# Performance work log

Hardware: AMD Instinct MI355X
Metric: run time of the kernel (lower is better)

Reference implementation:

```python
import jax, jax.numpy as jnp
import numpy as np

EMBED = 1024
HEADS = 16
HD = EMBED // HEADS
FF = 4096
EPS = 1e-5

def _layernorm(x, g, b):
    mu = jnp.mean(x, axis=-1, keepdims=True)
    var = jnp.mean(jnp.square(x - mu), axis=-1, keepdims=True)
    return (x - mu) * jax.lax.rsqrt(var + EPS) * g + b

def setup_inputs() -> dict:
    key = jax.random.key(0)
    ks = jax.random.split(key, 10)
    s = 0.02
    return {
        "x": jax.random.normal(ks[0], (4, 2048, EMBED), dtype=jnp.float32),
        "Wq": jax.random.normal(ks[1], (EMBED, EMBED), dtype=jnp.float32) * s,
        "Wk": jax.random.normal(ks[2], (EMBED, EMBED), dtype=jnp.float32) * s,
        "Wv": jax.random.normal(ks[3], (EMBED, EMBED), dtype=jnp.float32) * s,
        "Wo": jax.random.normal(ks[4], (EMBED, EMBED), dtype=jnp.float32) * s,
        "bo": jnp.zeros((EMBED,), dtype=jnp.float32),
        "W1": jax.random.normal(ks[5], (EMBED, FF), dtype=jnp.float32) * s,
        "b1": jnp.zeros((FF,), dtype=jnp.float32),
        "W2": jax.random.normal(ks[6], (FF, EMBED), dtype=jnp.float32) * s,
        "b2": jnp.zeros((EMBED,), dtype=jnp.float32),
        "g1": jnp.ones((EMBED,), dtype=jnp.float32),
        "be1": jnp.zeros((EMBED,), dtype=jnp.float32),
        "g2": jnp.ones((EMBED,), dtype=jnp.float32),
        "be2": jnp.zeros((EMBED,), dtype=jnp.float32),
    }

def reference(x, Wq, Wk, Wv, Wo, bo, W1, b1, W2, b2, g1, be1, g2, be2):
    B, T, _ = x.shape
    # --- pre-norm self-attention (dropout = identity in eval) ---
    h = _layernorm(x, g1, be1)
    q = (h @ Wq).reshape(B, T, HEADS, HD).transpose(0, 2, 1, 3)  # bhtd
    k = (h @ Wk).reshape(B, T, HEADS, HD).transpose(0, 2, 1, 3)
    v = (h @ Wv).reshape(B, T, HEADS, HD).transpose(0, 2, 1, 3)
    scores = jnp.einsum('bhid,bhjd->bhij', q, k) / jnp.sqrt(jnp.float32(HD))
    causal = jnp.tril(jnp.ones((T, T), dtype=bool))
    scores = jnp.where(causal[None, None], scores, -jnp.inf)
    attn = jax.nn.softmax(scores, axis=-1)
    out = jnp.einsum('bhij,bhjd->bhid', attn, v)
    out = out.transpose(0, 2, 1, 3).reshape(B, T, EMBED)
    out = out @ Wo + bo
    x = x + out
    # --- pre-norm GELU FFN ---
    h2 = _layernorm(x, g2, be2)
    ff = jax.nn.gelu(h2 @ W1 + b1, approximate=False) @ W2 + b2
    return x + ff
```

## Files before the change

kernel.cpp:

```cpp
#include <hip/hip_runtime.h>

typedef unsigned short u16;
typedef __attribute__((ext_vector_type(8))) short bf16x8;
typedef __attribute__((ext_vector_type(4))) float f32x4;

#define EMBED 1024
#define FFDIM 4096
#define SEQ   2048
#define NTOK  8192
#define ATT_C 0.18033688011112042f

__device__ __forceinline__ u16 f2bf(float f) {
  union { float f; unsigned int u; } c; c.f = f;
  unsigned int r = ((c.u >> 16) & 1u) + 0x7fffu;
  return (u16)((c.u + r) >> 16);
}

__device__ __forceinline__ unsigned cvtpk(float lo, float hi) {
  unsigned r;
  asm("v_cvt_pk_bf16_f32 %0, %1, %2" : "=v"(r) : "v"(lo), "v"(hi));
  return r;
}

__device__ __forceinline__ void gload16(const u16* g, u16* l) {
  __builtin_amdgcn_global_load_lds((const __attribute__((address_space(1))) void*)g,
                                   (__attribute__((address_space(3))) void*)l, 16, 0, 0);
}

__global__ __launch_bounds__(256) void wtrans(const float* __restrict__ W,
                                              u16* __restrict__ Wt, int K, int N) {
  __shared__ float tile[32][33];
  const int tx = threadIdx.x & 31, ty = threadIdx.x >> 5;
  const int n0 = blockIdx.x << 5, k0 = blockIdx.y << 5;
#pragma unroll
  for (int r = 0; r < 32; r += 8)
    tile[ty + r][tx] = W[(size_t)(k0 + ty + r) * N + n0 + tx];
  __syncthreads();
#pragma unroll
  for (int r = 0; r < 32; r += 8)
    Wt[(size_t)(n0 + ty + r) * K + k0 + tx] = f2bf(tile[tx][ty + r]);
}

__global__ __launch_bounds__(256) void vtrans(const u16* __restrict__ qkv,
                                              u16* __restrict__ Vt) {
  __shared__ u16 tile[32][33];
  const int tx = threadIdx.x & 31, ty = threadIdx.x >> 5;
  const int t0 = blockIdx.x << 5;
  const int rg0 = blockIdx.y << 5;
  const int bh = rg0 >> 6, d0 = rg0 & 63;
  const int b = bh >> 4, h = bh & 15;
#pragma unroll
  for (int r = 0; r < 32; r += 8)
    tile[ty + r][tx] = qkv[(size_t)(b * SEQ + t0 + ty + r) * 3072 + 2048 + h * 64 + d0 + tx];
  __syncthreads();
#pragma unroll
  for (int r = 0; r < 32; r += 8)
    Vt[(size_t)(rg0 + ty + r) * SEQ + t0 + tx] = tile[tx][ty + r];
}

__global__ __launch_bounds__(256) void ln_kernel(const float* __restrict__ xin,
                                                 const float* __restrict__ gamma,
                                                 const float* __restrict__ beta,
                                                 u16* __restrict__ out) {
  const int row = blockIdx.x, tid = threadIdx.x;
  const float4 v = reinterpret_cast<const float4*>(xin + (size_t)row * EMBED)[tid];
  float s  = v.x + v.y + v.z + v.w;
  float ss = v.x * v.x + v.y * v.y + v.z * v.z + v.w * v.w;
#pragma unroll
  for (int m = 1; m < 64; m <<= 1) { s += __shfl_xor(s, m); ss += __shfl_xor(ss, m); }
  __shared__ float red[8];
  if ((tid & 63) == 0) { red[tid >> 6] = s; red[4 + (tid >> 6)] = ss; }
  __syncthreads();
  s  = red[0] + red[1] + red[2] + red[3];
  ss = red[4] + red[5] + red[6] + red[7];
  const float mean = s * (1.0f / EMBED);
  const float var  = ss * (1.0f / EMBED) - mean * mean;
  const float rstd = rsqrtf(var + 1e-5f);
  const float4 g  = reinterpret_cast<const float4*>(gamma)[tid];
  const float4 bb = reinterpret_cast<const float4*>(beta)[tid];
  ushort4 o;
  o.x = f2bf((v.x - mean) * rstd * g.x + bb.x);
  o.y = f2bf((v.y - mean) * rstd * g.y + bb.y);
  o.z = f2bf((v.z - mean) * rstd * g.z + bb.z);
  o.w = f2bf((v.w - mean) * rstd * g.w + bb.w);
  reinterpret_cast<ushort4*>(out + (size_t)row * EMBED)[tid] = o;
}

template <int EPI>
__global__ __launch_bounds__(256) void gemm_bt(const u16* __restrict__ A,
                                               const u16* __restrict__ Bt,
                                               void* __restrict__ Cv,
                                               const float* __restrict__ bias,
                                               const float* __restrict__ res,
                                               int M, int N, int K) {
  __shared__ __align__(16) u16 As[128 * 64];
  __shared__ __align__(16) u16 Bs[128 * 64];
  const int tid = threadIdx.x;
  const int lane = tid & 63, wid = tid >> 6;
  const int l4 = lane >> 4, l15 = lane & 15;
  const int wr = wid >> 1, wc = wid & 1;

  const int gx = gridDim.x;
  const int nwg = gx * gridDim.y;
  const int flat = (int)blockIdx.y * gx + (int)blockIdx.x;
  const int cpx = nwg >> 3;
  const int swz = (flat & 7) * cpx + (flat >> 3);
  const int brow = (swz / gx) << 7, bcol = (swz % gx) << 7;

  const f32x4 z4 = {0.f, 0.f, 0.f, 0.f};
  f32x4 acc[4][4];
#pragma unroll
  for (int m = 0; m < 4; ++m)
#pragma unroll
    for (int n = 0; n < 4; ++n) acc[m][n] = z4;

  const int srow = tid >> 3;
  const int srck = ((tid & 7) << 4) ^ ((srow & 7) << 4);
  const u16* gA = A  + (size_t)(brow + srow) * K + (srck >> 1);
  const u16* gB = Bt + (size_t)(bcol + srow) * K + (srck >> 1);

  const int nk = K >> 6;
  for (int kt = 0; kt < nk; ++kt) {
    __syncthreads();
#pragma unroll
    for (int p = 0; p < 4; ++p) {
      gload16(gA + (size_t)p * 32 * K, &As[(p * 256 + wid * 64) * 8]);
      gload16(gB + (size_t)p * 32 * K, &Bs[(p * 256 + wid * 64) * 8]);
    }
    gA += 64; gB += 64;
    __syncthreads();
#pragma unroll
    for (int ks = 0; ks < 2; ++ks) {
      bf16x8 af[4], bfr[4];
      const int kk = ks * 32 + (l4 << 3);
#pragma unroll
      for (int m = 0; m < 4; ++m) {
        const int r = wr * 64 + m * 16 + l15;
        af[m] = *(const bf16x8*)&As[r * 64 + (kk ^ ((r & 7) << 3))];
      }
#pragma unroll
      for (int n = 0; n < 4; ++n) {
        const int r = wc * 64 + n * 16 + l15;
        bfr[n] = *(const bf16x8*)&Bs[r * 64 + (kk ^ ((r & 7) << 3))];
      }
#pragma unroll
      for (int m = 0; m < 4; ++m)
#pragma unroll
        for (int n = 0; n < 4; ++n)
          acc[m][n] = __builtin_amdgcn_mfma_f32_16x16x32_bf16(af[m], bfr[n], acc[m][n], 0, 0, 0);
    }
  }

  const int rowb = brow + wr * 64 + (l4 << 2);
  const int colb = bcol + wc * 64 + l15;
#pragma unroll
  for (int n = 0; n < 4; ++n) {
    const int col = colb + n * 16;
    float bv = 0.f;
    if (EPI != 0) bv = bias[col];
#pragma unroll
    for (int m = 0; m < 4; ++m) {
#pragma unroll
      for (int j = 0; j < 4; ++j) {
        const int row = rowb + m * 16 + j;
        const float v = acc[m][n][j];
        if (EPI == 0) {
          ((u16*)Cv)[(size_t)row * N + col] = f2bf(v);
        } else if (EPI == 1) {
          ((float*)Cv)[(size_t)row * N + col] = v + bv + res[(size_t)row * N + col];
        } else {
          const float t = v + bv;
          const float gl = 0.5f * t * (1.0f + erff(t * 0.70710678118654752f));
          ((u16*)Cv)[(size_t)row * N + col] = f2bf(gl);
        }
      }
    }
  }
}

__global__ __launch_bounds__(512) void attn_fwd(const u16* __restrict__ qkv,
                                                const u16* __restrict__ Vt,
                                                u16* __restrict__ attn) {
  __shared__ __align__(16) u16 Ks[64 * 72];
  __shared__ __align__(16) u16 Vs[64 * 72];
  __shared__ __align__(16) u16 Ps[8 * 16 * 72];
  const int tid = threadIdx.x, lane = tid & 63, wid = tid >> 6;
  const int l4 = lane >> 4, l15 = lane & 15;
  const int bh = blockIdx.y, b = bh >> 4, h = bh & 15;
  const size_t bt0 = (size_t)b * SEQ;
  u16* Pw = &Ps[wid * 16 * 72];

  const int sr = tid >> 3;
  const int sc0 = (tid & 7) << 3;
  const u16* kbase = qkv + bt0 * 3072 + 1024 + h * 64;
  const u16* vbase = Vt + (size_t)bh * 64 * SEQ;
  const f32x4 z4 = {0.f, 0.f, 0.f, 0.f};

#pragma unroll
  for (int ph = 0; ph < 2; ++ph) {
    const int Qb = ((ph == 0) ? (int)blockIdx.x : 15 - (int)blockIdx.x) << 7;
    const int qw = Qb + wid * 16;
    const int qlane = qw + l15;

    const u16* qp = qkv + (bt0 + qlane) * 3072 + h * 64 + (l4 << 3);
    const bf16x8 aq0 = *(const bf16x8*)qp;
    const bf16x8 aq1 = *(const bf16x8*)(qp + 32);

    f32x4 o[4];
#pragma unroll
    for (int dt = 0; dt < 4; ++dt) o[dt] = z4;
    float mrun = -1e30f, lrun = 0.f;

    bf16x8 kp = *(const bf16x8*)(kbase + (size_t)sr * 3072 + sc0);
    bf16x8 vp = *(const bf16x8*)(vbase + (size_t)sr * SEQ + sc0);

    const int jend = Qb + 128;
    for (int j0 = 0; j0 < jend; j0 += 64) {
      __syncthreads();
      *(bf16x8*)&Ks[sr * 72 + sc0] = kp;
      *(bf16x8*)&Vs[sr * 72 + sc0] = vp;
      __syncthreads();

      if (j0 + 64 < jend) {
        kp = *(const bf16x8*)(kbase + (size_t)(j0 + 64 + sr) * 3072 + sc0);
        vp = *(const bf16x8*)(vbase + (size_t)sr * SEQ + j0 + 64 + sc0);
      }

      if (j0 > qw + 15) continue;
      const int nt = min(4, ((qw + 15 - j0) >> 4) + 1);

      f32x4 s[4];
#pragma unroll
      for (int t = 0; t < 4; ++t) {
        if (t < nt) {
          const bf16x8 ak0 = *(const bf16x8*)&Ks[(t * 16 + l15) * 72 + (l4 << 3)];
          const bf16x8 ak1 = *(const bf16x8*)&Ks[(t * 16 + l15) * 72 + 32 + (l4 << 3)];
          f32x4 a = z4;
          a = __builtin_amdgcn_mfma_f32_16x16x32_bf16(ak0, aq0, a, 0, 0, 0);
          a = __builtin_amdgcn_mfma_f32_16x16x32_bf16(ak1, aq1, a, 0, 0, 0);
          s[t] = a;
        }
      }

      float mt = -1e30f;
#pragma unroll
      for (int t = 0; t < 4; ++t) {
        if (t < nt) {
          if (j0 + t * 16 + 15 > qw) {
            const int kvb = j0 + t * 16 + (l4 << 2);
#pragma unroll
            for (int j = 0; j < 4; ++j)
              if (kvb + j > qlane) s[t][j] = -1e30f;
          }
          mt = fmaxf(mt, fmaxf(fmaxf(s[t][0], s[t][1]), fmaxf(s[t][2], s[t][3])));
        }
      }
      mt = fmaxf(mt, __shfl_xor(mt, 16));
      mt = fmaxf(mt, __shfl_xor(mt, 32));

      const bool skip = __all(mt <= mrun + 44.0f);
      float scq = 1.0f;
      if (!skip) {
        const float mn = fmaxf(mrun, mt);
        scq = exp2f((mrun - mn) * ATT_C);
        mrun = mn;
      }
      const float mc = mrun * ATT_C;

      float ls = 0.f;
      uint2 pw[4];
#pragma unroll
      for (int t = 0; t < 4; ++t) {
        if (t < nt) {
          const float p0 = exp2f(__builtin_fmaf(s[t][0], ATT_C, -mc));
          const float p1 = exp2f(__builtin_fmaf(s[t][1], ATT_C, -mc));
          const float p2 = exp2f(__builtin_fmaf(s[t][2], ATT_C, -mc));
          const float p3 = exp2f(__builtin_fmaf(s[t][3], ATT_C, -mc));
          ls += (p0 + p1) + (p2 + p3);
          pw[t].x = cvtpk(p0, p1);
          pw[t].y = cvtpk(p2, p3);
        } else {
          pw[t].x = 0u; pw[t].y = 0u;
        }
      }
#pragma unroll
      for (int t = 0; t < 4; ++t)
        *(uint2*)&Pw[l15 * 72 + t * 16 + (l4 << 2)] = pw[t];

      ls += __shfl_xor(ls, 16);
      ls += __shfl_xor(ls, 32);

      if (!skip) {
        lrun = lrun * scq + ls;
#pragma unroll
        for (int dt = 0; dt < 4; ++dt)
#pragma unroll
          for (int j = 0; j < 4; ++j) o[dt][j] *= scq;
      } else {
        lrun += ls;
      }

      const int nc = (nt + 1) >> 1;
#pragma unroll
      for (int c = 0; c < 2; ++c) {
        if (c < nc) {
          const bf16x8 ap = *(const bf16x8*)&Pw[l15 * 72 + c * 32 + (l4 << 3)];
#pragma unroll
          for (int dt = 0; dt < 4; ++dt) {
            const bf16x8 bv = *(const bf16x8*)&Vs[(dt * 16 + l15) * 72 + c * 32 + (l4 << 3)];
            o[dt] = __builtin_amdgcn_mfma_f32_16x16x32_bf16(bv, ap, o[dt], 0, 0, 0);
          }
        }
      }
    }

    const float rl = 1.0f / lrun;
#pragma unroll
    for (int dt = 0; dt < 4; ++dt) {
      uint2 w;
      w.x = cvtpk(o[dt][0] * rl, o[dt][1] * rl);
      w.y = cvtpk(o[dt][2] * rl, o[dt][3] * rl);
      *(uint2*)&Pw[l15 * 72 + dt * 16 + (l4 << 2)] = w;
    }
#pragma unroll
    for (int rep = 0; rep < 2; ++rep) {
      const int unit = rep * 64 + lane;
      const int r = unit >> 3, c = unit & 7;
      const bf16x8 v = *(const bf16x8*)&Pw[r * 72 + c * 8];
      *(bf16x8*)&attn[(bt0 + qw + r) * EMBED + h * 64 + c * 8] = v;
    }
  }
}

extern "C" void kernel_launch(void* const* d_in, const int* in_sizes, int n_in,
                              void* d_out, int out_size, void* d_ws, size_t ws_size,
                              hipStream_t stream) {
  const float* x   = (const float*)d_in[0];
  const float* Wq  = (const float*)d_in[1];
  const float* Wk  = (const float*)d_in[2];
  const float* Wv  = (const float*)d_in[3];
  const float* Wo  = (const float*)d_in[4];
  const float* bo  = (const float*)d_in[5];
  const float* W1  = (const float*)d_in[6];
  const float* b1  = (const float*)d_in[7];
  const float* W2  = (const float*)d_in[8];
  const float* b2  = (const float*)d_in[9];
  const float* g1  = (const float*)d_in[10];
  const float* be1 = (const float*)d_in[11];
  const float* g2  = (const float*)d_in[12];
  const float* be2 = (const float*)d_in[13];

  char* ws = (char*)d_ws;
  u16* wqkv_t = (u16*)(ws + 0);
  u16* wo_t   = (u16*)(ws + 6291456);
  u16* w1_t   = (u16*)(ws + 8388608);
  u16* w2_t   = (u16*)(ws + 16777216);
  u16* hbuf   = (u16*)(ws + 25165824);
  u16* qkv    = (u16*)(ws + 41943040);
  u16* ff1    = (u16*)(ws + 41943040);
  u16* vt     = (u16*)(ws + 92274688);
  u16* attnb  = (u16*)(ws + 109051904);
  float* x2   = (float*)(ws + 125829120);
  float* outp = (float*)d_out;

  dim3 blk(256);
  wtrans<<<dim3(32, 32),  blk, 0, stream>>>(Wq, wqkv_t,               1024, 1024);
  wtrans<<<dim3(32, 32),  blk, 0, stream>>>(Wk, wqkv_t + 1024 * 1024, 1024, 1024);
  wtrans<<<dim3(32, 32),  blk, 0, stream>>>(Wv, wqkv_t + 2048 * 1024, 1024, 1024);
  wtrans<<<dim3(32, 32),  blk, 0, stream>>>(Wo, wo_t,                 1024, 1024);
  wtrans<<<dim3(128, 32), blk, 0, stream>>>(W1, w1_t,                 1024, 4096);
  wtrans<<<dim3(32, 128), blk, 0, stream>>>(W2, w2_t,                 4096, 1024);

  ln_kernel<<<dim3(8192), blk, 0, stream>>>(x, g1, be1, hbuf);
  gemm_bt<0><<<dim3(24, 64), blk, 0, stream>>>(hbuf, wqkv_t, qkv, nullptr, nullptr,
                                               8192, 3072, 1024);
  vtrans<<<dim3(64, 128), blk, 0, stream>>>(qkv, vt);
  attn_fwd<<<dim3(8, 64), dim3(512), 0, stream>>>(qkv, vt, attnb);
  gemm_bt<1><<<dim3(8, 64), blk, 0, stream>>>(attnb, wo_t, x2, bo, x,
                                              8192, 1024, 1024);
  ln_kernel<<<dim3(8192), blk, 0, stream>>>(x2, g2, be2, hbuf);
  gemm_bt<2><<<dim3(32, 64), blk, 0, stream>>>(hbuf, w1_t, ff1, b1, nullptr,
                                               8192, 4096, 1024);
  gemm_bt<1><<<dim3(8, 64), blk, 0, stream>>>(ff1, w2_t, outp, b2, x2,
                                              8192, 1024, 4096);
}
```

Measured before the change: 432.0 us.

## Replace GEMM with double-buffered 256-row tile kernel using 8 waves

Replaces the 128x128 single-buffered GEMM with a templated kernel that uses 256-row tiles, 128- or 256-column tiles and 512 threads. It double-buffers the LDS stages, prefetching the tile two steps ahead while MFMAs run, and uses explicit waitcnt, barriers and setprio to overlap loads with compute. The aim is to hide global-load latency and raise operand reuse per tile. In exchange it uses more LDS and registers, which limits occupancy, and the smaller grids for the N=1024 GEMMs may leave some CUs idle.

```diff
diff --git a/kernel.cpp b/kernel.cpp
--- a/kernel.cpp
+++ b/kernel.cpp
@@ -86,80 +86,132 @@
   reinterpret_cast<ushort4*>(out + (size_t)row * EMBED)[tid] = o;
 }
 
-template <int EPI>
-__global__ __launch_bounds__(256) void gemm_bt(const u16* __restrict__ A,
-                                               const u16* __restrict__ Bt,
-                                               void* __restrict__ Cv,
-                                               const float* __restrict__ bias,
-                                               const float* __restrict__ res,
-                                               int M, int N, int K) {
-  __shared__ __align__(16) u16 As[128 * 64];
-  __shared__ __align__(16) u16 Bs[128 * 64];
+template <int NREP, int EPI>
+__global__ __launch_bounds__(512, 2) void gemm2(const u16* __restrict__ A,
+                                                const u16* __restrict__ Bt,
+                                                void* __restrict__ Cv,
+                                                const float* __restrict__ bias,
+                                                const float* __restrict__ res,
+                                                int M, int N, int K) {
+  constexpr int BN = NREP * 64;
+  constexpr int TLOADS = 4 + NREP;
+  __shared__ __align__(16) u16 As[2][256 * 64];
+  __shared__ __align__(16) u16 Bs[2][BN * 64];
+
   const int tid = threadIdx.x;
   const int lane = tid & 63, wid = tid >> 6;
   const int l4 = lane >> 4, l15 = lane & 15;
-  const int wr = wid >> 1, wc = wid & 1;
+  const int wm = wid >> 2, wn = wid & 3;
 
   const int gx = gridDim.x;
-  const int nwg = gx * gridDim.y;
+  const int nwg = gx * (int)gridDim.y;
   const int flat = (int)blockIdx.y * gx + (int)blockIdx.x;
   const int cpx = nwg >> 3;
   const int swz = (flat & 7) * cpx + (flat >> 3);
-  const int brow = (swz / gx) << 7, bcol = (swz % gx) << 7;
+  const int brow = (swz / gx) << 8;
+  const int bcol = (swz % gx) * BN;
 
   const f32x4 z4 = {0.f, 0.f, 0.f, 0.f};
-  f32x4 acc[4][4];
-#pragma unroll
-  for (int m = 0; m < 4; ++m)
-#pragma unroll
-    for (int n = 0; n < 4; ++n) acc[m][n] = z4;
+  f32x4 acc[8][NREP];
+#pragma unroll
+  for (int m = 0; m < 8; ++m)
+#pragma unroll
+    for (int n = 0; n < NREP; ++n) acc[m][n] = z4;
 
   const int srow = tid >> 3;
-  const int srck = ((tid & 7) << 4) ^ ((srow & 7) << 4);
-  const u16* gA = A  + (size_t)(brow + srow) * K + (srck >> 1);
-  const u16* gB = Bt + (size_t)(bcol + srow) * K + (srck >> 1);
+  const int scolb = ((tid & 7) << 4) ^ ((srow & 7) << 4);
+  const u16* gA = A  + (size_t)(brow + srow) * K + (scolb >> 1);
+  const u16* gB = Bt + (size_t)(bcol + srow) * K + (scolb >> 1);
+  const int lbase = wid * 64 * 8;
 
   const int nk = K >> 6;
-  for (int kt = 0; kt < nk; ++kt) {
-    __syncthreads();
-#pragma unroll
-    for (int p = 0; p < 4; ++p) {
-      gload16(gA + (size_t)p * 32 * K, &As[(p * 256 + wid * 64) * 8]);
-      gload16(gB + (size_t)p * 32 * K, &Bs[(p * 256 + wid * 64) * 8]);
+
+#define STAGE(c, kt)                                                            \
+  do {                                                                          \
+    const u16* a_ = gA + (size_t)(kt) * 64;                                     \
+    const u16* b_ = gB + (size_t)(kt) * 64;                                     \
+    _Pragma("unroll")                                                           \
+    for (int k_ = 0; k_ < 4; ++k_)                                              \
+      gload16(a_ + (size_t)k_ * 64 * K, &As[c][lbase + k_ * 512 * 8]);          \
+    _Pragma("unroll")                                                           \
+    for (int k_ = 0; k_ < NREP; ++k_)                                           \
+      gload16(b_ + (size_t)k_ * 64 * K, &Bs[c][lbase + k_ * 512 * 8]);          \
+  } while (0)
+
+  STAGE(0, 0);
+  STAGE(1, 1);
+  asm volatile("s_waitcnt vmcnt(%0)" :: "i"(TLOADS) : "memory");
+  __builtin_amdgcn_sched_barrier(0);
+  __builtin_amdgcn_s_barrier();
+  __builtin_amdgcn_sched_barrier(0);
+
+  const int arow = wm * 128 + l15;
+  const int bcl  = wn * (BN / 4) + l15;
+  const int kk0  = l4 << 3;
+  const int aswz = (arow & 7) << 3;
+  const int bswz = (bcl & 7) << 3;
+
+  for (int t = 0; t < nk; ++t) {
+    const int c = t & 1;
+    const u16* as = As[c];
+    const u16* bs = Bs[c];
+    bf16x8 af[8], bf[NREP];
+
+#pragma unroll
+    for (int m = 0; m < 8; ++m)
+      af[m] = *(const bf16x8*)&as[(arow + m * 16) * 64 + (kk0 ^ aswz)];
+#pragma unroll
+    for (int n = 0; n < NREP; ++n)
+      bf[n] = *(const bf16x8*)&bs[(bcl + n * 16) * 64 + (kk0 ^ bswz)];
+    __builtin_amdgcn_s_setprio(1);
+#pragma unroll
+    for (int m = 0; m < 8; ++m)
+#pragma unroll
+      for (int n = 0; n < NREP; ++n)
+        acc[m][n] = __builtin_amdgcn_mfma_f32_16x16x32_bf16(af[m], bf[n], acc[m][n], 0, 0, 0);
+    __builtin_amdgcn_s_setprio(0);
+
+#pragma unroll
+    for (int m = 0; m < 8; ++m)
+      af[m] = *(const bf16x8*)&as[(arow + m * 16) * 64 + ((kk0 + 32) ^ aswz)];
+#pragma unroll
+    for (int n = 0; n < NREP; ++n)
+      bf[n] = *(const bf16x8*)&bs[(bcl + n * 16) * 64 + ((kk0 + 32) ^ bswz)];
+    asm volatile("s_waitcnt lgkmcnt(0)" ::: "memory");
+    __builtin_amdgcn_sched_barrier(0);
+    __builtin_amdgcn_s_barrier();
+    __builtin_amdgcn_sched_barrier(0);
+
+    if (t + 2 < nk) STAGE(c, t + 2);
+
+    __builtin_amdgcn_s_setprio(1);
+#pragma unroll
+    for (int m = 0; m < 8; ++m)
+#pragma unroll
+      for (int n = 0; n < NREP; ++n)
+        acc[m][n] = __builtin_amdgcn_mfma_f32_16x16x32_bf16(af[m], bf[n], acc[m][n], 0, 0, 0);
+    __builtin_amdgcn_s_setprio(0);
+
+    if (t + 2 < nk) {
+      asm volatile("s_waitcnt vmcnt(%0)" :: "i"(TLOADS) : "memory");
+    } else {
+      asm volatile("s_waitcnt vmcnt(0)" ::: "memory");
     }
-    gA += 64; gB += 64;
-    __syncthreads();
-#pragma unroll
-    for (int ks = 0; ks < 2; ++ks) {
-      bf16x8 af[4], bfr[4];
-      const int kk = ks * 32 + (l4 << 3);
-#pragma unroll
-      for (int m = 0; m < 4; ++m) {
-        const int r = wr * 64 + m * 16 + l15;
-        af[m] = *(const bf16x8*)&As[r * 64 + (kk ^ ((r & 7) << 3))];
-      }
-#pragma unroll
-      for (int n = 0; n < 4; ++n) {
-        const int r = wc * 64 + n * 16 + l15;
-        bfr[n] = *(const bf16x8*)&Bs[r * 64 + (kk ^ ((r & 7) << 3))];
-      }
-#pragma unroll
-      for (int m = 0; m < 4; ++m)
-#pragma unroll
-        for (int n = 0; n < 4; ++n)
-          acc[m][n] = __builtin_amdgcn_mfma_f32_16x16x32_bf16(af[m], bfr[n], acc[m][n], 0, 0, 0);
-    }
+    __builtin_amdgcn_sched_barrier(0);
+    __builtin_amdgcn_s_barrier();
+    __builtin_amdgcn_sched_barrier(0);
   }
-
-  const int rowb = brow + wr * 64 + (l4 << 2);
-  const int colb = bcol + wc * 64 + l15;
-#pragma unroll
-  for (int n = 0; n < 4; ++n) {
+#undef STAGE
+
+  const int rowb = brow + wm * 128 + (l4 << 2);
+  const int colb = bcol + wn * (BN / 4) + l15;
+#pragma unroll
+  for (int n = 0; n < NREP; ++n) {
     const int col = colb + n * 16;
     float bv = 0.f;
     if (EPI != 0) bv = bias[col];
 #pragma unroll
-    for (int m = 0; m < 4; ++m) {
+    for (int m = 0; m < 8; ++m) {
 #pragma unroll
       for (int j = 0; j < 4; ++j) {
         const int row = rowb + m * 16 + j;
@@ -169,8 +221,8 @@
         } else if (EPI == 1) {
           ((float*)Cv)[(size_t)row * N + col] = v + bv + res[(size_t)row * N + col];
         } else {
-          const float t = v + bv;
-          const float gl = 0.5f * t * (1.0f + erff(t * 0.70710678118654752f));
+          const float t2 = v + bv;
+          const float gl = 0.5f * t2 * (1.0f + erff(t2 * 0.70710678118654752f));
           ((u16*)Cv)[(size_t)row * N + col] = f2bf(gl);
         }
       }
@@ -372,15 +424,15 @@
   wtrans<<<dim3(32, 128), blk, 0, stream>>>(W2, w2_t,                 4096, 1024);
 
   ln_kernel<<<dim3(8192), blk, 0, stream>>>(x, g1, be1, hbuf);
-  gemm_bt<0><<<dim3(24, 64), blk, 0, stream>>>(hbuf, wqkv_t, qkv, nullptr, nullptr,
-                                               8192, 3072, 1024);
+  gemm2<4, 0><<<dim3(12, 32), dim3(512), 0, stream>>>(hbuf, wqkv_t, qkv, nullptr, nullptr,
+                                                      8192, 3072, 1024);
   vtrans<<<dim3(64, 128), blk, 0, stream>>>(qkv, vt);
   attn_fwd<<<dim3(8, 64), dim3(512), 0, stream>>>(qkv, vt, attnb);
-  gemm_bt<1><<<dim3(8, 64), blk, 0, stream>>>(attnb, wo_t, x2, bo, x,
-                                              8192, 1024, 1024);
+  gemm2<2, 1><<<dim3(8, 32), dim3(512), 0, stream>>>(attnb, wo_t, x2, bo, x,
+                                                     8192, 1024, 1024);
   ln_kernel<<<dim3(8192), blk, 0, stream>>>(x2, g2, be2, hbuf);
-  gemm_bt<2><<<dim3(32, 64), blk, 0, stream>>>(hbuf, w1_t, ff1, b1, nullptr,
-                                               8192, 4096, 1024);
-  gemm_bt<1><<<dim3(8, 64), blk, 0, stream>>>(ff1, w2_t, outp, b2, x2,
-                                              8192, 1024, 4096);
-}
+  gemm2<4, 2><<<dim3(16, 32), dim3(512), 0, stream>>>(hbuf, w1_t, ff1, b1, nullptr,
+                                                      8192, 4096, 1024);
+  gemm2<2, 1><<<dim3(8, 32), dim3(512), 0, stream>>>(ff1, w2_t, outp, b2, x2,
+                                                     8192, 1024, 4096);
+}
```

New measurement: 418.2 us. 1.03x faster.

## Replace GEMM with double-buffered 256-row tiled kernel using 8 waves and quadrant scheduling

Applied to the files above, without the earlier changes.

Replaces the 128x128 single-buffer GEMM with a 512-thread kernel that uses 256xBN tiles (BN of 128 or 256) and double-buffered LDS. Global loads for the next K tile are spread across four MFMA quadrant phases, using explicit waitcnt, barriers, sched_barrier and setprio to overlap memory traffic with MFMA work. The larger tiles raise data reuse per workgroup and cut redundant A/B traffic. The cost is much higher LDS and register use, which lowers occupancy, and fewer workgroups on the small-N GEMMs.

```diff
diff --git a/kernel.cpp b/kernel.cpp
--- a/kernel.cpp
+++ b/kernel.cpp
@@ -86,92 +86,190 @@
   reinterpret_cast<ushort4*>(out + (size_t)row * EMBED)[tid] = o;
 }
 
-template <int EPI>
-__global__ __launch_bounds__(256) void gemm_bt(const u16* __restrict__ A,
-                                               const u16* __restrict__ Bt,
-                                               void* __restrict__ Cv,
-                                               const float* __restrict__ bias,
-                                               const float* __restrict__ res,
-                                               int M, int N, int K) {
-  __shared__ __align__(16) u16 As[128 * 64];
-  __shared__ __align__(16) u16 Bs[128 * 64];
+template <int NREP, int EPI>
+__global__ __launch_bounds__(512, 2) void gemm4(const u16* __restrict__ A,
+                                                const u16* __restrict__ Bt,
+                                                void* __restrict__ Cv,
+                                                const float* __restrict__ bias,
+                                                const float* __restrict__ res,
+                                                int M, int N, int K) {
+  constexpr int BN = NREP * 64;
+  constexpr int G0 = 4;
+  constexpr int G1 = (NREP == 4) ? 4 : 3;
+  constexpr int G3 = (NREP == 4) ? 4 : 3;
+  constexpr int GP = (NREP == 4) ? 4 : 3;
+  __shared__ __align__(16) u16 As[2][256 * 64];
+  __shared__ __align__(16) u16 Bs[2][BN * 64];
+
   const int tid = threadIdx.x;
   const int lane = tid & 63, wid = tid >> 6;
   const int l4 = lane >> 4, l15 = lane & 15;
-  const int wr = wid >> 1, wc = wid & 1;
+  const int wq = wid >> 2, wn = wid & 3;
 
   const int gx = gridDim.x;
-  const int nwg = gx * gridDim.y;
+  const int nwg = gx * (int)gridDim.y;
   const int flat = (int)blockIdx.y * gx + (int)blockIdx.x;
   const int cpx = nwg >> 3;
   const int swz = (flat & 7) * cpx + (flat >> 3);
-  const int brow = (swz / gx) << 7, bcol = (swz % gx) << 7;
+  const int brow = (swz / gx) << 8;
+  const int bcol = (swz % gx) * BN;
 
   const f32x4 z4 = {0.f, 0.f, 0.f, 0.f};
-  f32x4 acc[4][4];
-#pragma unroll
-  for (int m = 0; m < 4; ++m)
-#pragma unroll
-    for (int n = 0; n < 4; ++n) acc[m][n] = z4;
+  f32x4 acc[4][4][NREP / 2];
+#pragma unroll
+  for (int q = 0; q < 4; ++q)
+#pragma unroll
+    for (int m = 0; m < 4; ++m)
+#pragma unroll
+      for (int n = 0; n < NREP / 2; ++n) acc[q][m][n] = z4;
 
   const int srow = tid >> 3;
-  const int srck = ((tid & 7) << 4) ^ ((srow & 7) << 4);
-  const u16* gA = A  + (size_t)(brow + srow) * K + (srck >> 1);
-  const u16* gB = Bt + (size_t)(bcol + srow) * K + (srck >> 1);
+  const int scolb = ((tid & 7) << 4) ^ ((srow & 7) << 4);
+  const u16* gAs = A  + (size_t)(brow + srow) * K + (scolb >> 1);
+  const u16* gBs = Bt + (size_t)(bcol + srow) * K + (scolb >> 1);
+  const int lA = wid * 512;
 
   const int nk = K >> 6;
-  for (int kt = 0; kt < nk; ++kt) {
-    __syncthreads();
-#pragma unroll
-    for (int p = 0; p < 4; ++p) {
-      gload16(gA + (size_t)p * 32 * K, &As[(p * 256 + wid * 64) * 8]);
-      gload16(gB + (size_t)p * 32 * K, &Bs[(p * 256 + wid * 64) * 8]);
-    }
-    gA += 64; gB += 64;
-    __syncthreads();
-#pragma unroll
-    for (int ks = 0; ks < 2; ++ks) {
-      bf16x8 af[4], bfr[4];
-      const int kk = ks * 32 + (l4 << 3);
+
+#define STAGE_A(c_, t_, h_)                                                     \
+  do {                                                                          \
+    gload16(gAs + (size_t)((h_) * 128) * K + (size_t)(t_) * 64,                 \
+            &As[c_][(h_) * 8192 + lA]);                                         \
+    gload16(gAs + (size_t)((h_) * 128 + 64) * K + (size_t)(t_) * 64,            \
+            &As[c_][(h_) * 8192 + 4096 + lA]);                                  \
+  } while (0)
+#define STAGE_B(c_, t_, h_)                                                     \
+  do {                                                                          \
+    if constexpr (NREP == 4) {                                                  \
+      gload16(gBs + (size_t)((h_) * 128) * K + (size_t)(t_) * 64,               \
+              &Bs[c_][(h_) * 8192 + lA]);                                       \
+      gload16(gBs + (size_t)((h_) * 128 + 64) * K + (size_t)(t_) * 64,          \
+              &Bs[c_][(h_) * 8192 + 4096 + lA]);                                \
+    } else {                                                                    \
+      gload16(gBs + (size_t)((h_) * 64) * K + (size_t)(t_) * 64,                \
+              &Bs[c_][(h_) * 4096 + lA]);                                       \
+    }                                                                           \
+  } while (0)
+
+#define SB __builtin_amdgcn_sched_barrier(0)
+#define BARR do { SB; __builtin_amdgcn_s_barrier(); SB; } while (0)
+#define LG0  do { asm volatile("s_waitcnt lgkmcnt(0)" ::: "memory"); SB; } while (0)
+#define VM(N_) do { asm volatile("s_waitcnt vmcnt(%0)" :: "i"(N_) : "memory"); SB; } while (0)
+
+  const int kk0  = l4 << 3;
+  const int aswz = (l15 & 7) << 3;
+
+#define RD_A(MH)                                                                \
+  _Pragma("unroll")                                                             \
+  for (int m_ = 0; m_ < 4; ++m_)                                                \
+    _Pragma("unroll")                                                           \
+    for (int ks_ = 0; ks_ < 2; ++ks_)                                           \
+      af[m_][ks_] = *(const bf16x8*)&As[c][((MH) * 128 + wq * 64 + m_ * 16 + l15) * 64 + ((kk0 + ks_ * 32) ^ aswz)];
+#define RD_B(NH)                                                                \
+  _Pragma("unroll")                                                             \
+  for (int n_ = 0; n_ < NREP / 2; ++n_)                                         \
+    _Pragma("unroll")                                                           \
+    for (int ks_ = 0; ks_ < 2; ++ks_)                                           \
+      bf[n_][ks_] = *(const bf16x8*)&Bs[c][((NH) * (BN / 2) + wn * (BN / 8) + n_ * 16 + l15) * 64 + ((kk0 + ks_ * 32) ^ aswz)];
+#define MFMA_Q(Q_)                                                              \
+  __builtin_amdgcn_s_setprio(1);                                                \
+  _Pragma("unroll")                                                             \
+  for (int m_ = 0; m_ < 4; ++m_)                                                \
+    _Pragma("unroll")                                                           \
+    for (int n_ = 0; n_ < NREP / 2; ++n_)                                       \
+      _Pragma("unroll")                                                         \
+      for (int ks_ = 0; ks_ < 2; ++ks_)                                         \
+        acc[Q_][m_][n_] = __builtin_amdgcn_mfma_f32_16x16x32_bf16(              \
+            af[m_][ks_], bf[n_][ks_], acc[Q_][m_][n_], 0, 0, 0);                \
+  __builtin_amdgcn_s_setprio(0);
+
+  bf16x8 af[4][2], bf[NREP / 2][2];
+
+  STAGE_A(0, 0, 0);
+  STAGE_B(0, 0, 0);
+  STAGE_B(0, 0, 1);
+  STAGE_A(0, 0, 1);
+  VM(GP);
+  BARR;
+
+  for (int t = 0; t < nk - 1; ++t) {
+    const int c = t & 1, cn = c ^ 1;
+    RD_A(0); RD_B(0);
+    STAGE_A(cn, t + 1, 0);
+    BARR; LG0;
+    MFMA_Q(0);
+    VM(G0); BARR;
+    RD_B(1);
+    STAGE_B(cn, t + 1, 0);
+    BARR; LG0;
+    MFMA_Q(1);
+    VM(G1); BARR;
+    RD_A(1);
+    STAGE_B(cn, t + 1, 1);
+    BARR; LG0;
+    MFMA_Q(2);
+    BARR;
+    RD_B(0);
+    STAGE_A(cn, t + 1, 1);
+    BARR; LG0;
+    MFMA_Q(3);
+    VM(G3); BARR;
+  }
+
+  {
+    const int c = (nk - 1) & 1;
+    RD_A(0); RD_B(0);
+    BARR; LG0;
+    MFMA_Q(0);
+    VM(2); BARR;
+    RD_B(1);
+    BARR; LG0;
+    MFMA_Q(1);
+    VM(0); BARR;
+    RD_A(1);
+    BARR; LG0;
+    MFMA_Q(2);
+    BARR;
+    RD_B(0);
+    LG0;
+    MFMA_Q(3);
+  }
+
+#undef STAGE_A
+#undef STAGE_B
+#undef SB
+#undef BARR
+#undef LG0
+#undef VM
+#undef RD_A
+#undef RD_B
+#undef MFMA_Q
+
+#pragma unroll
+  for (int q = 0; q < 4; ++q) {
+    const int mh = q >> 1, nh = (q >> 1) ^ (q & 1);
+    const int rowb = brow + mh * 128 + wq * 64 + (l4 << 2);
+    const int colb = bcol + nh * (BN / 2) + wn * (BN / 8) + l15;
+#pragma unroll
+    for (int n = 0; n < NREP / 2; ++n) {
+      const int col = colb + n * 16;
+      float bv = 0.f;
+      if (EPI != 0) bv = bias[col];
 #pragma unroll
       for (int m = 0; m < 4; ++m) {
-        const int r = wr * 64 + m * 16 + l15;
-        af[m] = *(const bf16x8*)&As[r * 64 + (kk ^ ((r & 7) << 3))];
-      }
-#pragma unroll
-      for (int n = 0; n < 4; ++n) {
-        const int r = wc * 64 + n * 16 + l15;
-        bfr[n] = *(const bf16x8*)&Bs[r * 64 + (kk ^ ((r & 7) << 3))];
-      }
-#pragma unroll
-      for (int m = 0; m < 4; ++m)
-#pragma unroll
-        for (int n = 0; n < 4; ++n)
-          acc[m][n] = __builtin_amdgcn_mfma_f32_16x16x32_bf16(af[m], bfr[n], acc[m][n], 0, 0, 0);
-    }
-  }
-
-  const int rowb = brow + wr * 64 + (l4 << 2);
-  const int colb = bcol + wc * 64 + l15;
-#pragma unroll
-  for (int n = 0; n < 4; ++n) {
-    const int col = colb + n * 16;
-    float bv = 0.f;
-    if (EPI != 0) bv = bias[col];
-#pragma unroll
-    for (int m = 0; m < 4; ++m) {
-#pragma unroll
-      for (int j = 0; j < 4; ++j) {
-        const int row = rowb + m * 16 + j;
-        const float v = acc[m][n][j];
-        if (EPI == 0) {
-          ((u16*)Cv)[(size_t)row * N + col] = f2bf(v);
-        } else if (EPI == 1) {
-          ((float*)Cv)[(size_t)row * N + col] = v + bv + res[(size_t)row * N + col];
-        } else {
-          const float t = v + bv;
-          const float gl = 0.5f * t * (1.0f + erff(t * 0.70710678118654752f));
-          ((u16*)Cv)[(size_t)row * N + col] = f2bf(gl);
+#pragma unroll
+        for (int j = 0; j < 4; ++j) {
+          const int row = rowb + m * 16 + j;
+          const float v = acc[q][m][n][j];
+          if (EPI == 0) {
+            ((u16*)Cv)[(size_t)row * N + col] = f2bf(v);
+          } else if (EPI == 1) {
+            ((float*)Cv)[(size_t)row * N + col] = v + bv + res[(size_t)row * N + col];
+          } else {
+            const float t2 = v + bv;
+            const float gl = 0.5f * t2 * (1.0f + erff(t2 * 0.70710678118654752f));
+            ((u16*)Cv)[(size_t)row * N + col] = f2bf(gl);
+          }
         }
       }
     }
@@ -372,15 +470,15 @@
   wtrans<<<dim3(32, 128), blk, 0, stream>>>(W2, w2_t,                 4096, 1024);
 
   ln_kernel<<<dim3(8192), blk, 0, stream>>>(x, g1, be1, hbuf);
-  gemm_bt<0><<<dim3(24, 64), blk, 0, stream>>>(hbuf, wqkv_t, qkv, nullptr, nullptr,
-                                               8192, 3072, 1024);
+  gemm4<2, 0><<<dim3(24, 32), dim3(512), 0, stream>>>(hbuf, wqkv_t, qkv, nullptr, nullptr,
+                                                      8192, 3072, 1024);
   vtrans<<<dim3(64, 128), blk, 0, stream>>>(qkv, vt);
   attn_fwd<<<dim3(8, 64), dim3(512), 0, stream>>>(qkv, vt, attnb);
-  gemm_bt<1><<<dim3(8, 64), blk, 0, stream>>>(attnb, wo_t, x2, bo, x,
-                                              8192, 1024, 1024);
+  gemm4<2, 1><<<dim3(8, 32), dim3(512), 0, stream>>>(attnb, wo_t, x2, bo, x,
+                                                     8192, 1024, 1024);
   ln_kernel<<<dim3(8192), blk, 0, stream>>>(x2, g2, be2, hbuf);
-  gemm_bt<2><<<dim3(32, 64), blk, 0, stream>>>(hbuf, w1_t, ff1, b1, nullptr,
-                                               8192, 4096, 1024);
-  gemm_bt<1><<<dim3(8, 64), blk, 0, stream>>>(ff1, w2_t, outp, b2, x2,
-                                              8192, 1024, 4096);
-}
+  gemm4<4, 2><<<dim3(16, 32), dim3(512), 0, stream>>>(hbuf, w1_t, ff1, b1, nullptr,
+                                                      8192, 4096, 1024);
+  gemm4<2, 1><<<dim3(8, 32), dim3(512), 0, stream>>>(ff1, w2_t, outp, b2, x2,
+                                                     8192, 1024, 4096);
+}
```

Result: slower. 455.9 us, median of 4 (+5.5%).
